# Performance work log

Measured on AMD Instinct MI355X. Metric: run time of the kernel, lower is better.

Reference implementation:

```python
import jax, jax.numpy as jnp
import numpy as np

N, E = 100000, 1600000
NODE_IN, EDGE_IN, H = 128, 16, 128


def sage_conv(x, src, dst, Wl, Wr, b, n_nodes):
    # PyG SAGEConv (aggr='mean'): out = lin_l(mean_{j->i} x_j) + lin_r(x_i), bias on lin_l
    msg_sum = jax.ops.segment_sum(x[src], dst, num_segments=n_nodes)      # [N, d]
    cnt = jax.ops.segment_sum(jnp.ones((src.shape[0],), x.dtype), dst, num_segments=n_nodes)
    mean = msg_sum / jnp.maximum(cnt, 1.0)[:, None]                        # empty neighborhoods -> 0
    return mean @ Wl + x @ Wr + b


def setup_inputs() -> dict:
    key = jax.random.key(0)
    ks = jax.random.split(key, 12)
    s = lambda d: 1.0 / np.sqrt(d)
    return {
        "x": jax.random.normal(ks[0], (N, NODE_IN), jnp.float32),
        "edge_index": jax.random.randint(ks[1], (2, E), 0, N, dtype=jnp.int64),
        "edge_attr": jax.random.normal(ks[2], (E, EDGE_IN), jnp.float32),
        "Wl1": jax.random.normal(ks[3], (NODE_IN, H), jnp.float32) * s(NODE_IN),
        "Wr1": jax.random.normal(ks[4], (NODE_IN, H), jnp.float32) * s(NODE_IN),
        "b1": jnp.zeros((H,), jnp.float32),
        "Wl2": jax.random.normal(ks[5], (H, H), jnp.float32) * s(H),
        "Wr2": jax.random.normal(ks[6], (H, H), jnp.float32) * s(H),
        "b2": jnp.zeros((H,), jnp.float32),
        "Wm1": jax.random.normal(ks[7], (2 * H + EDGE_IN, H), jnp.float32) * s(2 * H + EDGE_IN),
        "bm1": jnp.zeros((H,), jnp.float32),
        "Wm2": jax.random.normal(ks[8], (H, 1), jnp.float32) * s(H),
        "bm2": jnp.zeros((1,), jnp.float32),
    }


def reference(x, edge_index, edge_attr, Wl1, Wr1, b1, Wl2, Wr2, b2, Wm1, bm1, Wm2, bm2):
    src, dst = edge_index[0], edge_index[1]
    h = jax.nn.relu(sage_conv(x, src, dst, Wl1, Wr1, b1, N))
    h = jax.nn.relu(sage_conv(h, src, dst, Wl2, Wr2, b2, N))
    edge_feat = jnp.concatenate([h[src], h[dst], edge_attr], axis=1)  # [E, 2H+edge_in]
    out = jax.nn.relu(edge_feat @ Wm1 + bm1) @ Wm2 + bm2               # dropout is identity in eval
    return out.reshape(-1)
```

## Files before the change

kernel.cpp:

```cpp
#include <hip/hip_runtime.h>

typedef _Float16 f16;
typedef _Float16 f16x8 __attribute__((ext_vector_type(8)));
typedef float f32x4 __attribute__((ext_vector_type(4)));

#define MFMA16(a,b,c) __builtin_amdgcn_mfma_f32_16x16x32_f16((a),(b),(c),0,0,0)

__global__ void k_detect(const long long* ei, int n_nodes, int* flag) {
    long long v = ei[threadIdx.x];
    int bad = (v < 0 || v >= n_nodes);
    unsigned long long m = __ballot(bad);
    if (threadIdx.x == 0) *flag = (m == 0ULL);
}

__global__ void k_idx(const void* ei, int E, const int* __restrict__ flag,
                      int* __restrict__ src, int* __restrict__ dst) {
    int e = blockIdx.x * 256 + threadIdx.x;
    if (e >= E) return;
    if (*flag) {
        const long long* p = (const long long*)ei;
        src[e] = (int)p[e];
        dst[e] = (int)p[(size_t)E + e];
    } else {
        const int* p = (const int*)ei;
        src[e] = p[e];
        dst[e] = p[(size_t)E + e];
    }
}

__global__ void k_x2h(const float* __restrict__ x, f16* __restrict__ xh, int n) {
    int i = (blockIdx.x * 256 + threadIdx.x) * 8;
    if (i >= n) return;
    float4 a = *(const float4*)(x + i);
    float4 b = *(const float4*)(x + i + 4);
    f16x8 h;
    h[0] = (f16)a.x; h[1] = (f16)a.y; h[2] = (f16)a.z; h[3] = (f16)a.w;
    h[4] = (f16)b.x; h[5] = (f16)b.y; h[6] = (f16)b.z; h[7] = (f16)b.w;
    *(f16x8*)(xh + i) = h;
}

__global__ void k_wfrag(const float* __restrict__ Wa, const float* __restrict__ Wb,
                        f16* __restrict__ dst, int KS) {
    int t = blockIdx.x * 256 + threadIdx.x;
    int total = KS * 8 * 64;
    if (t >= total) return;
    int l = t & 63;
    int s = t >> 9;
    int k0 = s * 32 + (l >> 4) * 8;
    int j = ((t >> 6) & 7) * 16 + (l & 15);
    f16x8 h;
    #pragma unroll
    for (int e = 0; e < 8; e++) {
        int k = k0 + e;
        float v = (k < 128) ? Wa[k * 128 + j] : Wb[(k - 128) * 128 + j];
        h[e] = (f16)v;
    }
    *(f16x8*)(dst + (size_t)t * 8) = h;
}

__global__ void k_zfrag(const float* __restrict__ Wm1, f16* __restrict__ dst) {
    int t = blockIdx.x * 256 + threadIdx.x;
    if (t >= 4 * 16 * 64) return;
    int lane = t & 63, c = (t >> 6) & 15, s = t >> 10;
    int k0 = s * 32 + (lane >> 4) * 8;
    int j = c * 16 + (lane & 15);
    f16x8 h;
    #pragma unroll
    for (int e = 0; e < 8; e++) {
        int k = k0 + e;
        float v = (j < 128) ? Wm1[k * 128 + j] : Wm1[(128 + k) * 128 + (j - 128)];
        h[e] = (f16)v;
    }
    *(f16x8*)(dst + (size_t)t * 8) = h;
}

__global__ void k_wefrag(const float* __restrict__ Wm1, f16* __restrict__ dst) {
    int t = blockIdx.x * 256 + threadIdx.x;
    if (t >= 8 * 64) return;
    int lane = t & 63, ct = t >> 6;
    int k0 = (lane >> 4) * 8;
    int j = ct * 16 + (lane & 15);
    f16x8 h;
    #pragma unroll
    for (int e = 0; e < 8; e++) {
        int k = k0 + e;
        h[e] = (k < 16) ? (f16)Wm1[(256 + k) * 128 + j] : (f16)0.0f;
    }
    *(f16x8*)(dst + (size_t)t * 8) = h;
}

__global__ void k_hist(const int* __restrict__ dst, int E, int* __restrict__ deg) {
    int e = blockIdx.x * 256 + threadIdx.x;
    if (e < E) atomicAdd(&deg[dst[e]], 1);
}

__global__ void k_bsum(const int* __restrict__ deg, int n, int* __restrict__ bsum) {
    __shared__ int ws[4];
    const int tid = threadIdx.x;
    int i = blockIdx.x * 1024 + tid * 4;
    int s = 0;
    if (i + 3 < n) {
        int4 d = *(const int4*)(deg + i);
        s = d.x + d.y + d.z + d.w;
    } else {
        #pragma unroll
        for (int j = 0; j < 4; j++) if (i + j < n) s += deg[i + j];
    }
    #pragma unroll
    for (int m = 1; m < 64; m <<= 1) s += __shfl_xor(s, m, 64);
    if ((tid & 63) == 0) ws[tid >> 6] = s;
    __syncthreads();
    if (tid == 0) bsum[blockIdx.x] = ws[0] + ws[1] + ws[2] + ws[3];
}

__global__ void k_bscan(int* __restrict__ bsum, int nb, int* __restrict__ rowptr_n) {
    __shared__ int wsum[4];
    const int tid = threadIdx.x, lane = tid & 63, wid = tid >> 6;
    int v = (tid < nb) ? bsum[tid] : 0;
    int inc = v;
    #pragma unroll
    for (int off = 1; off < 64; off <<= 1) {
        int u = __shfl_up(inc, off, 64);
        if (lane >= off) inc += u;
    }
    if (lane == 63) wsum[wid] = inc;
    __syncthreads();
    int woff = 0;
    for (int j = 0; j < wid; j++) woff += wsum[j];
    int excl = woff + inc - v;
    if (tid < nb) bsum[tid] = excl;
    if (tid == nb - 1) rowptr_n[0] = excl + v;
}

__global__ void k_rowptr(const int* __restrict__ deg, int n, const int* __restrict__ boff,
                         int* __restrict__ rowptr, int* __restrict__ cursor) {
    __shared__ int wsum[4];
    const int tid = threadIdx.x, lane = tid & 63, wid = tid >> 6;
    int i = blockIdx.x * 1024 + tid * 4;
    int d0 = 0, d1 = 0, d2 = 0, d3 = 0;
    if (i + 3 < n) {
        int4 d = *(const int4*)(deg + i);
        d0 = d.x; d1 = d.y; d2 = d.z; d3 = d.w;
    } else {
        if (i     < n) d0 = deg[i];
        if (i + 1 < n) d1 = deg[i + 1];
        if (i + 2 < n) d2 = deg[i + 2];
        if (i + 3 < n) d3 = deg[i + 3];
    }
    int s = d0 + d1 + d2 + d3;
    int inc = s;
    #pragma unroll
    for (int off = 1; off < 64; off <<= 1) {
        int u = __shfl_up(inc, off, 64);
        if (lane >= off) inc += u;
    }
    if (lane == 63) wsum[wid] = inc;
    __syncthreads();
    int woff = 0;
    for (int j = 0; j < wid; j++) woff += wsum[j];
    int excl = boff[blockIdx.x] + woff + inc - s;
    int e1 = excl + d0, e2 = e1 + d1, e3 = e2 + d2;
    if (i     < n) { rowptr[i]     = excl; cursor[i]     = excl; }
    if (i + 1 < n) { rowptr[i + 1] = e1;   cursor[i + 1] = e1; }
    if (i + 2 < n) { rowptr[i + 2] = e2;   cursor[i + 2] = e2; }
    if (i + 3 < n) { rowptr[i + 3] = e3;   cursor[i + 3] = e3; }
}

__global__ void k_scatter(const int* __restrict__ src, const int* __restrict__ dst, int E,
                          int* __restrict__ cursor, int* __restrict__ col) {
    int e = blockIdx.x * 256 + threadIdx.x;
    if (e < E) {
        int p = atomicAdd(&cursor[dst[e]], 1);
        col[p] = src[e];
    }
}

#define AP 136
template<int DO_Z>
__global__ __launch_bounds__(256, DO_Z ? 3 : 4) void k_fuse(
    const f16* __restrict__ tab,
    const int* __restrict__ rowptr, const int* __restrict__ col,
    const f16* __restrict__ Wf, const float* __restrict__ bias,
    const f16* __restrict__ zwf, const float* __restrict__ bm1,
    f16* __restrict__ out, int n_rows) {
    __shared__ __align__(16) f16 sA[64 * AP];
    const int tid = threadIdx.x, lane = tid & 63, w = tid >> 6;
    const int l15 = lane & 15, g = lane >> 4;
    const int base = blockIdx.x * 64;

    const int g16 = tid >> 4, c = tid & 15;
    #pragma unroll
    for (int rep = 0; rep < 4; rep++) {
        const int node = base + rep * 16 + g16;
        float acc[8] = {0.f, 0.f, 0.f, 0.f, 0.f, 0.f, 0.f, 0.f};
        int d = 1;
        if (node < n_rows) {
            const int s0 = rowptr[node], s1 = rowptr[node + 1];
            int k = s0;
            for (; k + 3 < s1; k += 4) {
                const int n0 = col[k], n1 = col[k + 1], n2 = col[k + 2], n3 = col[k + 3];
                f16x8 v0 = *(const f16x8*)(tab + (size_t)n0 * 128 + c * 8);
                f16x8 v1 = *(const f16x8*)(tab + (size_t)n1 * 128 + c * 8);
                f16x8 v2 = *(const f16x8*)(tab + (size_t)n2 * 128 + c * 8);
                f16x8 v3 = *(const f16x8*)(tab + (size_t)n3 * 128 + c * 8);
                #pragma unroll
                for (int j = 0; j < 8; j++)
                    acc[j] += ((float)v0[j] + (float)v1[j]) + ((float)v2[j] + (float)v3[j]);
            }
            for (; k < s1; ++k) {
                const int n0 = col[k];
                f16x8 v0 = *(const f16x8*)(tab + (size_t)n0 * 128 + c * 8);
                #pragma unroll
                for (int j = 0; j < 8; j++) acc[j] += (float)v0[j];
            }
            d = s1 - s0; if (d < 1) d = 1;
        }
        const float inv = 1.f / (float)d;
        f16x8 r;
        #pragma unroll
        for (int j = 0; j < 8; j++) r[j] = (f16)(acc[j] * inv);
        *(f16x8*)&sA[(rep * 16 + g16) * AP + c * 8] = r;
    }
    __syncthreads();

    const int c0 = (2 * w) * 16 + l15, c1 = c0 + 16;
    const float b0 = bias[c0], b1 = bias[c1];
    f32x4 acc[4][2];
    #pragma unroll
    for (int t = 0; t < 4; t++) {
        acc[t][0] = f32x4{b0, b0, b0, b0};
        acc[t][1] = f32x4{b1, b1, b1, b1};
    }
    #pragma unroll
    for (int s = 0; s < 8; s++) {
        f16x8 bf0 = *(const f16x8*)&Wf[((size_t)(s * 8 + 2 * w    ) * 64 + lane) * 8];
        f16x8 bf1 = *(const f16x8*)&Wf[((size_t)(s * 8 + 2 * w + 1) * 64 + lane) * 8];
        const int koff = (s & 3) * 32 + g * 8;
        #pragma unroll
        for (int t = 0; t < 4; t++) {
            f16x8 a;
            if (s < 4) {
                a = *(const f16x8*)&sA[(t * 16 + l15) * AP + koff];
            } else {
                int row = base + t * 16 + l15;
                if (row >= n_rows) row = n_rows - 1;
                a = *(const f16x8*)(tab + (size_t)row * 128 + koff);
            }
            acc[t][0] = MFMA16(a, bf0, acc[t][0]);
            acc[t][1] = MFMA16(a, bf1, acc[t][1]);
        }
    }

    if (DO_Z == 0) {
        #pragma unroll
        for (int t = 0; t < 4; t++) {
            #pragma unroll
            for (int i = 0; i < 4; i++) {
                int row = base + t * 16 + g * 4 + i;
                if (row < n_rows) {
                    float v0 = acc[t][0][i]; v0 = v0 > 0.f ? v0 : 0.f;
                    float v1 = acc[t][1][i]; v1 = v1 > 0.f ? v1 : 0.f;
                    out[(size_t)row * 128 + c0] = (f16)v0;
                    out[(size_t)row * 128 + c1] = (f16)v1;
                }
            }
        }
    } else {
        __syncthreads();
        #pragma unroll
        for (int t = 0; t < 4; t++) {
            #pragma unroll
            for (int i = 0; i < 4; i++) {
                const int rl = t * 16 + g * 4 + i;
                float v0 = acc[t][0][i]; v0 = v0 > 0.f ? v0 : 0.f;
                float v1 = acc[t][1][i]; v1 = v1 > 0.f ? v1 : 0.f;
                sA[rl * AP + c0] = (f16)v0;
                sA[rl * AP + c1] = (f16)v1;
            }
        }
        __syncthreads();
        #pragma unroll
        for (int half = 0; half < 2; half++) {
            const int j0 = (4 * w + 2 * half) * 16 + l15, j1 = j0 + 16;
            const float zb0 = (j0 >= 128) ? bm1[j0 - 128] : 0.0f;
            const float zb1 = (j1 >= 128) ? bm1[j1 - 128] : 0.0f;
            f32x4 zacc[4][2];
            #pragma unroll
            for (int t = 0; t < 4; t++) {
                zacc[t][0] = f32x4{zb0, zb0, zb0, zb0};
                zacc[t][1] = f32x4{zb1, zb1, zb1, zb1};
            }
            #pragma unroll
            for (int s = 0; s < 4; s++) {
                f16x8 wf0 = *(const f16x8*)&zwf[((size_t)(s * 16 + 4 * w + 2 * half    ) * 64 + lane) * 8];
                f16x8 wf1 = *(const f16x8*)&zwf[((size_t)(s * 16 + 4 * w + 2 * half + 1) * 64 + lane) * 8];
                const int koff = s * 32 + g * 8;
                #pragma unroll
                for (int t = 0; t < 4; t++) {
                    f16x8 a = *(const f16x8*)&sA[(t * 16 + l15) * AP + koff];
                    zacc[t][0] = MFMA16(a, wf0, zacc[t][0]);
                    zacc[t][1] = MFMA16(a, wf1, zacc[t][1]);
                }
            }
            #pragma unroll
            for (int t = 0; t < 4; t++) {
                #pragma unroll
                for (int i = 0; i < 4; i++) {
                    int row = base + t * 16 + g * 4 + i;
                    if (row < n_rows) {
                        out[(size_t)row * 256 + j0] = (f16)zacc[t][0][i];
                        out[(size_t)row * 256 + j1] = (f16)zacc[t][1][i];
                    }
                }
            }
        }
    }
}

#define ZP 136
__global__ __launch_bounds__(256, 4) void k_edge2(
    const f16* __restrict__ z, const float* __restrict__ ea,
    const int* __restrict__ src, const int* __restrict__ dst,
    const f16* __restrict__ wef, const float* __restrict__ Wm2,
    const float* __restrict__ bm2, float* __restrict__ out,
    int E, int iters, int gridW) {
    __shared__ __align__(16) f16 sZ[64 * ZP];
    __shared__ __align__(16) f16 sEA[4 * 64 * 8];
    __shared__ float sPart[4][64];
    const int tid = threadIdx.x, lane = tid & 63, w = tid >> 6;
    const int l15 = lane & 15, g = lane >> 4;
    const int sr = lane >> 2, sq = lane & 3;
    const int slot_s = w * 16 + sr;

    for (int i = tid; i < 4 * 64; i += 256)
        *(f16x8*)(&sEA[0] + (size_t)i * 8) = f16x8{};

    const f16x8 be0 = *(const f16x8*)(wef + ((size_t)((2 * w) * 64 + lane)) * 8);
    const f16x8 be1 = *(const f16x8*)(wef + ((size_t)((2 * w + 1) * 64 + lane)) * 8);
    const float w20 = Wm2[(2 * w) * 16 + l15];
    const float w21 = Wm2[(2 * w + 1) * 16 + l15];
    const float bv = bm2[0];

    f16x8 zs[4], zd[4];
    union { f16 h[4]; uint2 u2; } eh;

    auto stage_load = [&](int ebase) {
        int er = ebase + slot_s; if (er > E - 1) er = E - 1;
        const int is = src[er], id = dst[er];
        const f16* ps = z + (size_t)is * 256 + sq * 32;
        const f16* pd = z + (size_t)id * 256 + 128 + sq * 32;
        #pragma unroll
        for (int i = 0; i < 4; i++) {
            zs[i] = *(const f16x8*)(ps + i * 8);
            zd[i] = *(const f16x8*)(pd + i * 8);
        }
        float4 ev = *(const float4*)(ea + (size_t)er * 16 + sq * 4);
        eh.h[0] = (f16)ev.x; eh.h[1] = (f16)ev.y; eh.h[2] = (f16)ev.z; eh.h[3] = (f16)ev.w;
    };
    auto stage_write = [&]() {
        f16* zp = &sZ[0] + slot_s * ZP + sq * 32;
        #pragma unroll
        for (int i = 0; i < 4; i++) {
            f16x8 v = zs[i] + zd[i];
            *(f16x8*)(zp + i * 8) = v;
        }
        f16* ep = &sEA[0] +
                  ((size_t)((slot_s >> 4) * 64 + (sq >> 1) * 16 + (slot_s & 15)) * 8 + (sq & 1) * 4);
        *(uint2*)ep = eh.u2;
    };

    stage_load(blockIdx.x * 64);
    __syncthreads();
    stage_write();
    __syncthreads();

    for (int it = 0; it < iters; ++it) {
        const int ebase = (blockIdx.x + it * gridW) * 64;
        if (ebase >= E) break;
        const int nxt = (blockIdx.x + (it + 1) * gridW) * 64;
        const bool has_next = (it + 1 < iters) && (nxt < E);
        if (has_next) stage_load(nxt);

        f32x4 acc[4][2];
        #pragma unroll
        for (int t = 0; t < 4; t++) { acc[t][0] = f32x4{0,0,0,0}; acc[t][1] = f32x4{0,0,0,0}; }
        #pragma unroll
        for (int t = 0; t < 4; t++) {
            f16x8 a = *(const f16x8*)(&sEA[0] + ((size_t)(t * 64 + lane)) * 8);
            acc[t][0] = MFMA16(a, be0, acc[t][0]);
            acc[t][1] = MFMA16(a, be1, acc[t][1]);
        }
        #pragma unroll
        for (int t = 0; t < 4; t++) {
            float p[4];
            #pragma unroll
            for (int i = 0; i < 4; i++) {
                int slot = t * 16 + g * 4 + i;
                float z0 = (float)sZ[slot * ZP + (2 * w) * 16 + l15];
                float z1 = (float)sZ[slot * ZP + (2 * w + 1) * 16 + l15];
                float v0 = z0 + acc[t][0][i]; v0 = v0 > 0.f ? v0 : 0.f;
                float v1 = z1 + acc[t][1][i]; v1 = v1 > 0.f ? v1 : 0.f;
                p[i] = v0 * w20 + v1 * w21;
            }
            #pragma unroll
            for (int m = 1; m < 16; m <<= 1)
                #pragma unroll
                for (int i = 0; i < 4; i++) p[i] += __shfl_xor(p[i], m, 64);
            if (l15 == 0)
                #pragma unroll
                for (int i = 0; i < 4; i++) sPart[w][t * 16 + g * 4 + i] = p[i];
        }
        __syncthreads();
        if (tid < 64) {
            int e = ebase + tid;
            if (e < E)
                out[e] = sPart[0][tid] + sPart[1][tid] + sPart[2][tid] + sPart[3][tid] + bv;
        }
        if (has_next) stage_write();
        __syncthreads();
    }
}

extern "C" void kernel_launch(void* const* d_in, const int* in_sizes, int n_in,
                              void* d_out, int out_size, void* d_ws, size_t ws_size,
                              hipStream_t stream) {
    const float* x   = (const float*)d_in[0];
    const void*  ei  = d_in[1];
    const float* ea  = (const float*)d_in[2];
    const float* Wl1 = (const float*)d_in[3];
    const float* Wr1 = (const float*)d_in[4];
    const float* b1  = (const float*)d_in[5];
    const float* Wl2 = (const float*)d_in[6];
    const float* Wr2 = (const float*)d_in[7];
    const float* b2  = (const float*)d_in[8];
    const float* Wm1 = (const float*)d_in[9];
    const float* bm1 = (const float*)d_in[10];
    const float* Wm2 = (const float*)d_in[11];
    const float* bm2 = (const float*)d_in[12];

    const int N = in_sizes[0] / 128;
    const int E = in_sizes[1] / 2;

    char* ws = (char*)d_ws;
    size_t off = 0;
    auto alloc = [&](size_t bytes) -> void* {
        void* p = ws + off;
        off = (off + bytes + 255) & ~(size_t)255;
        return p;
    };
    f16* z      = (f16*)alloc((size_t)N * 256 * 2);
    f16* xh     = z;
    f16* h1     = (f16*)alloc((size_t)N * 128 * 2);
    int* src    = (int*)alloc((size_t)E * 4);
    int* dst    = (int*)alloc((size_t)E * 4);
    int* col    = (int*)alloc((size_t)E * 4);
    int* deg    = (int*)alloc((size_t)N * 4);
    int* rowptr = (int*)alloc((size_t)(N + 1) * 4);
    int* cursor = (int*)alloc((size_t)N * 4);
    int* bsum   = (int*)alloc((size_t)1024 * 4);
    f16* w1f    = (f16*)alloc((size_t)8 * 8 * 64 * 8 * 2);
    f16* w2f    = (f16*)alloc((size_t)8 * 8 * 64 * 8 * 2);
    f16* zwf    = (f16*)alloc((size_t)4 * 16 * 64 * 8 * 2);
    f16* wef    = (f16*)alloc((size_t)8 * 64 * 8 * 2);
    int* flag   = (int*)alloc(4);
    if (off > ws_size) return;

    const int eb = (E + 255) / 256;
    const int nbk = (N + 1023) / 1024;
    const int rb64 = (N + 63) / 64;

    k_detect<<<1, 64, 0, stream>>>((const long long*)ei, N, flag);
    k_idx<<<eb, 256, 0, stream>>>(ei, E, flag, src, dst);
    k_x2h<<<(N * 128 / 8 + 255) / 256, 256, 0, stream>>>(x, xh, N * 128);
    k_wfrag<<<16, 256, 0, stream>>>(Wl1, Wr1, w1f, 8);
    k_wfrag<<<16, 256, 0, stream>>>(Wl2, Wr2, w2f, 8);
    k_zfrag<<<16, 256, 0, stream>>>(Wm1, zwf);
    k_wefrag<<<2, 256, 0, stream>>>(Wm1, wef);

    hipMemsetAsync(deg, 0, (size_t)N * 4, stream);
    k_hist<<<eb, 256, 0, stream>>>(dst, E, deg);
    k_bsum<<<nbk, 256, 0, stream>>>(deg, N, bsum);
    k_bscan<<<1, 256, 0, stream>>>(bsum, nbk, rowptr + N);
    k_rowptr<<<nbk, 256, 0, stream>>>(deg, N, bsum, rowptr, cursor);
    k_scatter<<<eb, 256, 0, stream>>>(src, dst, E, cursor, col);

    k_fuse<0><<<rb64, 256, 0, stream>>>(xh, rowptr, col, w1f, b1, nullptr, nullptr, h1, N);
    k_fuse<1><<<rb64, 256, 0, stream>>>(h1, rowptr, col, w2f, b2, zwf, bm1, z, N);

    const int eg = 1792;
    const int nb = (E + 63) / 64;
    const int e_iters = (nb + eg - 1) / eg;
    k_edge2<<<eg, 256, 0, stream>>>(z, ea, src, dst, wef, Wm2, bm2,
                                    (float*)d_out, E, e_iters, eg);
}
```

Measured before the change: 570.8 us.

## Split aggregation from GEMM and use chunked column-slab layout for node features

Node features are stored as 8 column slabs of 16 halves ([chunk][N][16]) instead of row-major 128-wide rows. Neighbor aggregation becomes its own kernel that handles one slab per block, so each pass gathers from a 3.2 MB slab that can stay cache-resident rather than a full 25.6 MB table. The SAGE GEMMs then read the mean and self features from the slab layout. This adds a mean buffer, extra kernel launches and a round trip of the mean through global memory, and makes the self-feature A-loads 32-byte strided pieces.

Measured after the change: 608.9 us. 6.7% more time.

```diff
diff --git a/kernel.cpp b/kernel.cpp
--- a/kernel.cpp
+++ b/kernel.cpp
@@ -5,6 +5,7 @@
 typedef float f32x4 __attribute__((ext_vector_type(4)));
 
 #define MFMA16(a,b,c) __builtin_amdgcn_mfma_f32_16x16x32_f16((a),(b),(c),0,0,0)
+
 
 __global__ void k_detect(const long long* ei, int n_nodes, int* flag) {
     long long v = ei[threadIdx.x];
@@ -28,15 +29,18 @@
     }
 }
 
-__global__ void k_x2h(const float* __restrict__ x, f16* __restrict__ xh, int n) {
-    int i = (blockIdx.x * 256 + threadIdx.x) * 8;
-    if (i >= n) return;
-    float4 a = *(const float4*)(x + i);
-    float4 b = *(const float4*)(x + i + 4);
+__global__ void k_x2h(const float* __restrict__ x, f16* __restrict__ xs, int N) {
+    int i = blockIdx.x * 256 + threadIdx.x;
+    if (i >= N * 16) return;
+    int n = i >> 4, cg = i & 15;
+    const float* px = x + (size_t)n * 128 + cg * 8;
+    float4 a = *(const float4*)px;
+    float4 b = *(const float4*)(px + 4);
     f16x8 h;
     h[0] = (f16)a.x; h[1] = (f16)a.y; h[2] = (f16)a.z; h[3] = (f16)a.w;
     h[4] = (f16)b.x; h[5] = (f16)b.y; h[6] = (f16)b.z; h[7] = (f16)b.w;
-    *(f16x8*)(xh + i) = h;
+    int chunk = cg >> 1, off = (cg & 1) * 8;
+    *(f16x8*)(xs + ((size_t)chunk * N + n) * 16 + off) = h;
 }
 
 __global__ void k_wfrag(const float* __restrict__ Wa, const float* __restrict__ Wb,
@@ -175,56 +179,101 @@
     }
 }
 
+__global__ __launch_bounds__(256) void k_aggs(
+    const f16* __restrict__ tabs, const int* __restrict__ rowptr,
+    const int* __restrict__ col, f16* __restrict__ means, int N) {
+    const int chunk = blockIdx.x & 7;
+    const int tile = blockIdx.x >> 3;
+    const int team = threadIdx.x >> 1, half = threadIdx.x & 1;
+    const int node = tile * 128 + team;
+    if (node >= N) return;
+    const f16* slab = tabs + (size_t)chunk * N * 16 + half * 8;
+    const int s0 = rowptr[node], s1 = rowptr[node + 1];
+    float acc[8] = {0.f, 0.f, 0.f, 0.f, 0.f, 0.f, 0.f, 0.f};
+    int k = s0;
+    for (; k + 3 < s1; k += 4) {
+        const int n0 = col[k], n1 = col[k + 1], n2 = col[k + 2], n3 = col[k + 3];
+        f16x8 v0 = *(const f16x8*)(slab + (size_t)n0 * 16);
+        f16x8 v1 = *(const f16x8*)(slab + (size_t)n1 * 16);
+        f16x8 v2 = *(const f16x8*)(slab + (size_t)n2 * 16);
+        f16x8 v3 = *(const f16x8*)(slab + (size_t)n3 * 16);
+        #pragma unroll
+        for (int j = 0; j < 8; j++)
+            acc[j] += ((float)v0[j] + (float)v1[j]) + ((float)v2[j] + (float)v3[j]);
+    }
+    for (; k < s1; ++k) {
+        const int n0 = col[k];
+        f16x8 v0 = *(const f16x8*)(slab + (size_t)n0 * 16);
+        #pragma unroll
+        for (int j = 0; j < 8; j++) acc[j] += (float)v0[j];
+    }
+    int d = s1 - s0; if (d < 1) d = 1;
+    const float inv = 1.f / (float)d;
+    f16x8 r;
+    #pragma unroll
+    for (int j = 0; j < 8; j++) r[j] = (f16)(acc[j] * inv);
+    *(f16x8*)(means + ((size_t)chunk * N + node) * 16 + half * 8) = r;
+}
+
+__global__ __launch_bounds__(256) void k_gemm2(
+    const f16* __restrict__ As, const f16* __restrict__ Ss,
+    const f16* __restrict__ Wf, const float* __restrict__ bias,
+    f16* __restrict__ outs, int N) {
+    const int tid = threadIdx.x, lane = tid & 63, w = tid >> 6;
+    const int l15 = lane & 15, g = lane >> 4;
+    const int base = blockIdx.x * 64;
+    const int c0 = (2 * w) * 16 + l15, c1 = c0 + 16;
+    const float b0 = bias[c0], b1 = bias[c1];
+    const int chp = g >> 1, off = (g & 1) * 8;
+    f32x4 acc[4][2];
+    #pragma unroll
+    for (int t = 0; t < 4; t++) {
+        acc[t][0] = f32x4{b0, b0, b0, b0};
+        acc[t][1] = f32x4{b1, b1, b1, b1};
+    }
+    #pragma unroll
+    for (int s = 0; s < 8; s++) {
+        f16x8 bf0 = *(const f16x8*)&Wf[((size_t)(s * 8 + 2 * w    ) * 64 + lane) * 8];
+        f16x8 bf1 = *(const f16x8*)&Wf[((size_t)(s * 8 + 2 * w + 1) * 64 + lane) * 8];
+        const f16* Asrc = (s < 4) ? As : Ss;
+        const int chunk = (s & 3) * 2 + chp;
+        #pragma unroll
+        for (int t = 0; t < 4; t++) {
+            int row = base + t * 16 + l15;
+            if (row >= N) row = N - 1;
+            f16x8 a = *(const f16x8*)(Asrc + ((size_t)chunk * N + row) * 16 + off);
+            acc[t][0] = MFMA16(a, bf0, acc[t][0]);
+            acc[t][1] = MFMA16(a, bf1, acc[t][1]);
+        }
+    }
+    #pragma unroll
+    for (int t = 0; t < 4; t++) {
+        #pragma unroll
+        for (int i = 0; i < 4; i++) {
+            int row = base + t * 16 + g * 4 + i;
+            if (row < N) {
+                float v0 = acc[t][0][i]; v0 = v0 > 0.f ? v0 : 0.f;
+                float v1 = acc[t][1][i]; v1 = v1 > 0.f ? v1 : 0.f;
+                outs[((size_t)(2 * w    ) * N + row) * 16 + l15] = (f16)v0;
+                outs[((size_t)(2 * w + 1) * N + row) * 16 + l15] = (f16)v1;
+            }
+        }
+    }
+}
+
 #define AP 136
-template<int DO_Z>
-__global__ __launch_bounds__(256, DO_Z ? 3 : 4) void k_fuse(
-    const f16* __restrict__ tab,
-    const int* __restrict__ rowptr, const int* __restrict__ col,
+__global__ __launch_bounds__(256, 3) void k_gemmz(
+    const f16* __restrict__ As, const f16* __restrict__ Ss,
     const f16* __restrict__ Wf, const float* __restrict__ bias,
     const f16* __restrict__ zwf, const float* __restrict__ bm1,
-    f16* __restrict__ out, int n_rows) {
+    f16* __restrict__ z, int N) {
     __shared__ __align__(16) f16 sA[64 * AP];
     const int tid = threadIdx.x, lane = tid & 63, w = tid >> 6;
     const int l15 = lane & 15, g = lane >> 4;
     const int base = blockIdx.x * 64;
-
-    const int g16 = tid >> 4, c = tid & 15;
-    #pragma unroll
-    for (int rep = 0; rep < 4; rep++) {
-        const int node = base + rep * 16 + g16;
-        float acc[8] = {0.f, 0.f, 0.f, 0.f, 0.f, 0.f, 0.f, 0.f};
-        int d = 1;
-        if (node < n_rows) {
-            const int s0 = rowptr[node], s1 = rowptr[node + 1];
-            int k = s0;
-            for (; k + 3 < s1; k += 4) {
-                const int n0 = col[k], n1 = col[k + 1], n2 = col[k + 2], n3 = col[k + 3];
-                f16x8 v0 = *(const f16x8*)(tab + (size_t)n0 * 128 + c * 8);
-                f16x8 v1 = *(const f16x8*)(tab + (size_t)n1 * 128 + c * 8);
-                f16x8 v2 = *(const f16x8*)(tab + (size_t)n2 * 128 + c * 8);
-                f16x8 v3 = *(const f16x8*)(tab + (size_t)n3 * 128 + c * 8);
-                #pragma unroll
-                for (int j = 0; j < 8; j++)
-                    acc[j] += ((float)v0[j] + (float)v1[j]) + ((float)v2[j] + (float)v3[j]);
-            }
-            for (; k < s1; ++k) {
-                const int n0 = col[k];
-                f16x8 v0 = *(const f16x8*)(tab + (size_t)n0 * 128 + c * 8);
-                #pragma unroll
-                for (int j = 0; j < 8; j++) acc[j] += (float)v0[j];
-            }
-            d = s1 - s0; if (d < 1) d = 1;
-        }
-        const float inv = 1.f / (float)d;
-        f16x8 r;
-        #pragma unroll
-        for (int j = 0; j < 8; j++) r[j] = (f16)(acc[j] * inv);
-        *(f16x8*)&sA[(rep * 16 + g16) * AP + c * 8] = r;
-    }
-    __syncthreads();
-
     const int c0 = (2 * w) * 16 + l15, c1 = c0 + 16;
     const float b0 = bias[c0], b1 = bias[c1];
+    const int chp = g >> 1, off = (g & 1) * 8;
     f32x4 acc[4][2];
     #pragma unroll
     for (int t = 0; t < 4; t++) {
@@ -235,82 +284,60 @@
     for (int s = 0; s < 8; s++) {
         f16x8 bf0 = *(const f16x8*)&Wf[((size_t)(s * 8 + 2 * w    ) * 64 + lane) * 8];
         f16x8 bf1 = *(const f16x8*)&Wf[((size_t)(s * 8 + 2 * w + 1) * 64 + lane) * 8];
-        const int koff = (s & 3) * 32 + g * 8;
+        const f16* Asrc = (s < 4) ? As : Ss;
+        const int chunk = (s & 3) * 2 + chp;
         #pragma unroll
         for (int t = 0; t < 4; t++) {
-            f16x8 a;
-            if (s < 4) {
-                a = *(const f16x8*)&sA[(t * 16 + l15) * AP + koff];
-            } else {
-                int row = base + t * 16 + l15;
-                if (row >= n_rows) row = n_rows - 1;
-                a = *(const f16x8*)(tab + (size_t)row * 128 + koff);
-            }
+            int row = base + t * 16 + l15;
+            if (row >= N) row = N - 1;
+            f16x8 a = *(const f16x8*)(Asrc + ((size_t)chunk * N + row) * 16 + off);
             acc[t][0] = MFMA16(a, bf0, acc[t][0]);
             acc[t][1] = MFMA16(a, bf1, acc[t][1]);
         }
     }
-
-    if (DO_Z == 0) {
+    #pragma unroll
+    for (int t = 0; t < 4; t++) {
+        #pragma unroll
+        for (int i = 0; i < 4; i++) {
+            const int rl = t * 16 + g * 4 + i;
+            float v0 = acc[t][0][i]; v0 = v0 > 0.f ? v0 : 0.f;
+            float v1 = acc[t][1][i]; v1 = v1 > 0.f ? v1 : 0.f;
+            sA[rl * AP + c0] = (f16)v0;
+            sA[rl * AP + c1] = (f16)v1;
+        }
+    }
+    __syncthreads();
+    #pragma unroll
+    for (int half = 0; half < 2; half++) {
+        const int j0 = (4 * w + 2 * half) * 16 + l15, j1 = j0 + 16;
+        const float zb0 = (j0 >= 128) ? bm1[j0 - 128] : 0.0f;
+        const float zb1 = (j1 >= 128) ? bm1[j1 - 128] : 0.0f;
+        f32x4 zacc[4][2];
+        #pragma unroll
+        for (int t = 0; t < 4; t++) {
+            zacc[t][0] = f32x4{zb0, zb0, zb0, zb0};
+            zacc[t][1] = f32x4{zb1, zb1, zb1, zb1};
+        }
+        #pragma unroll
+        for (int s = 0; s < 4; s++) {
+            f16x8 wf0 = *(const f16x8*)&zwf[((size_t)(s * 16 + 4 * w + 2 * half    ) * 64 + lane) * 8];
+            f16x8 wf1 = *(const f16x8*)&zwf[((size_t)(s * 16 + 4 * w + 2 * half + 1) * 64 + lane) * 8];
+            const int koff = s * 32 + g * 8;
+            #pragma unroll
+            for (int t = 0; t < 4; t++) {
+                f16x8 a = *(const f16x8*)&sA[(t * 16 + l15) * AP + koff];
+                zacc[t][0] = MFMA16(a, wf0, zacc[t][0]);
+                zacc[t][1] = MFMA16(a, wf1, zacc[t][1]);
+            }
+        }
         #pragma unroll
         for (int t = 0; t < 4; t++) {
             #pragma unroll
             for (int i = 0; i < 4; i++) {
                 int row = base + t * 16 + g * 4 + i;
-                if (row < n_rows) {
-                    float v0 = acc[t][0][i]; v0 = v0 > 0.f ? v0 : 0.f;
-                    float v1 = acc[t][1][i]; v1 = v1 > 0.f ? v1 : 0.f;
-                    out[(size_t)row * 128 + c0] = (f16)v0;
-                    out[(size_t)row * 128 + c1] = (f16)v1;
-                }
-            }
-        }
-    } else {
-        __syncthreads();
-        #pragma unroll
-        for (int t = 0; t < 4; t++) {
-            #pragma unroll
-            for (int i = 0; i < 4; i++) {
-                const int rl = t * 16 + g * 4 + i;
-                float v0 = acc[t][0][i]; v0 = v0 > 0.f ? v0 : 0.f;
-                float v1 = acc[t][1][i]; v1 = v1 > 0.f ? v1 : 0.f;
-                sA[rl * AP + c0] = (f16)v0;
-                sA[rl * AP + c1] = (f16)v1;
-            }
-        }
-        __syncthreads();
-        #pragma unroll
-        for (int half = 0; half < 2; half++) {
-            const int j0 = (4 * w + 2 * half) * 16 + l15, j1 = j0 + 16;
-            const float zb0 = (j0 >= 128) ? bm1[j0 - 128] : 0.0f;
-            const float zb1 = (j1 >= 128) ? bm1[j1 - 128] : 0.0f;
-            f32x4 zacc[4][2];
-            #pragma unroll
-            for (int t = 0; t < 4; t++) {
-                zacc[t][0] = f32x4{zb0, zb0, zb0, zb0};
-                zacc[t][1] = f32x4{zb1, zb1, zb1, zb1};
-            }
-            #pragma unroll
-            for (int s = 0; s < 4; s++) {
-                f16x8 wf0 = *(const f16x8*)&zwf[((size_t)(s * 16 + 4 * w + 2 * half    ) * 64 + lane) * 8];
-                f16x8 wf1 = *(const f16x8*)&zwf[((size_t)(s * 16 + 4 * w + 2 * half + 1) * 64 + lane) * 8];
-                const int koff = s * 32 + g * 8;
-                #pragma unroll
-                for (int t = 0; t < 4; t++) {
-                    f16x8 a = *(const f16x8*)&sA[(t * 16 + l15) * AP + koff];
-                    zacc[t][0] = MFMA16(a, wf0, zacc[t][0]);
-                    zacc[t][1] = MFMA16(a, wf1, zacc[t][1]);
-                }
-            }
-            #pragma unroll
-            for (int t = 0; t < 4; t++) {
-                #pragma unroll
-                for (int i = 0; i < 4; i++) {
-                    int row = base + t * 16 + g * 4 + i;
-                    if (row < n_rows) {
-                        out[(size_t)row * 256 + j0] = (f16)zacc[t][0][i];
-                        out[(size_t)row * 256 + j1] = (f16)zacc[t][1][i];
-                    }
+                if (row < N) {
+                    z[(size_t)row * 256 + j0] = (f16)zacc[t][0][i];
+                    z[(size_t)row * 256 + j1] = (f16)zacc[t][1][i];
                 }
             }
         }
@@ -451,6 +478,7 @@
     f16* z      = (f16*)alloc((size_t)N * 256 * 2);
     f16* xh     = z;
     f16* h1     = (f16*)alloc((size_t)N * 128 * 2);
+    f16* mean   = (f16*)alloc((size_t)N * 128 * 2);
     int* src    = (int*)alloc((size_t)E * 4);
     int* dst    = (int*)alloc((size_t)E * 4);
     int* col    = (int*)alloc((size_t)E * 4);
@@ -471,7 +499,7 @@
 
     k_detect<<<1, 64, 0, stream>>>((const long long*)ei, N, flag);
     k_idx<<<eb, 256, 0, stream>>>(ei, E, flag, src, dst);
-    k_x2h<<<(N * 128 / 8 + 255) / 256, 256, 0, stream>>>(x, xh, N * 128);
+    k_x2h<<<(N * 16 + 255) / 256, 256, 0, stream>>>(x, xh, N);
     k_wfrag<<<16, 256, 0, stream>>>(Wl1, Wr1, w1f, 8);
     k_wfrag<<<16, 256, 0, stream>>>(Wl2, Wr2, w2f, 8);
     k_zfrag<<<16, 256, 0, stream>>>(Wm1, zwf);
@@ -484,8 +512,12 @@
     k_rowptr<<<nbk, 256, 0, stream>>>(deg, N, bsum, rowptr, cursor);
     k_scatter<<<eb, 256, 0, stream>>>(src, dst, E, cursor, col);
 
-    k_fuse<0><<<rb64, 256, 0, stream>>>(xh, rowptr, col, w1f, b1, nullptr, nullptr, h1, N);
-    k_fuse<1><<<rb64, 256, 0, stream>>>(h1, rowptr, col, w2f, b2, zwf, bm1, z, N);
+    const int ag = 8 * ((N + 127) / 128);
+
+    k_aggs<<<ag, 256, 0, stream>>>(xh, rowptr, col, mean, N);
+    k_gemm2<<<rb64, 256, 0, stream>>>(mean, xh, w1f, b1, h1, N);
+    k_aggs<<<ag, 256, 0, stream>>>(h1, rowptr, col, mean, N);
+    k_gemmz<<<rb64, 256, 0, stream>>>(mean, h1, w2f, b2, zwf, bm1, z, N);
 
     const int eg = 1792;
     const int nb = (E + 63) / 64;
```

## Process edges in CSR (dst-sorted) order in edge MLP, then permute outputs

Applied to the files above, without the earlier changes.

The edge MLP kernel now walks edges in the dst-sorted CSR order built by the scatter pass, so consecutive edges share destination rows of z and hit cache better. The scatter pass records the original edge id and destination per slot, and a new permutation kernel writes results back to original order. The degree histogram is also folded into the index conversion kernel, dropping one launch and one read of dst. In exchange, edge_attr reads become gathers, and the change adds extra index arrays, a temporary output buffer and a scattered write pass.

Result: faster. 559.1 us (-2.1%).

```diff
diff --git a/kernel.cpp b/kernel.cpp
--- a/kernel.cpp
+++ b/kernel.cpp
@@ -14,18 +14,23 @@
 }
 
 __global__ void k_idx(const void* ei, int E, const int* __restrict__ flag,
-                      int* __restrict__ src, int* __restrict__ dst) {
+                      int* __restrict__ src, int* __restrict__ dst,
+                      int* __restrict__ deg) {
     int e = blockIdx.x * 256 + threadIdx.x;
     if (e >= E) return;
+    int s, d;
     if (*flag) {
         const long long* p = (const long long*)ei;
-        src[e] = (int)p[e];
-        dst[e] = (int)p[(size_t)E + e];
+        s = (int)p[e];
+        d = (int)p[(size_t)E + e];
     } else {
         const int* p = (const int*)ei;
-        src[e] = p[e];
-        dst[e] = p[(size_t)E + e];
-    }
+        s = p[e];
+        d = p[(size_t)E + e];
+    }
+    src[e] = s;
+    dst[e] = d;
+    atomicAdd(&deg[d], 1);
 }
 
 __global__ void k_x2h(const float* __restrict__ x, f16* __restrict__ xh, int n) {
@@ -87,11 +92,6 @@
         h[e] = (k < 16) ? (f16)Wm1[(256 + k) * 128 + j] : (f16)0.0f;
     }
     *(f16x8*)(dst + (size_t)t * 8) = h;
-}
-
-__global__ void k_hist(const int* __restrict__ dst, int E, int* __restrict__ deg) {
-    int e = blockIdx.x * 256 + threadIdx.x;
-    if (e < E) atomicAdd(&deg[dst[e]], 1);
 }
 
 __global__ void k_bsum(const int* __restrict__ deg, int n, int* __restrict__ bsum) {
@@ -167,11 +167,15 @@
 }
 
 __global__ void k_scatter(const int* __restrict__ src, const int* __restrict__ dst, int E,
-                          int* __restrict__ cursor, int* __restrict__ col) {
+                          int* __restrict__ cursor, int* __restrict__ col,
+                          int* __restrict__ eid, int* __restrict__ dstp) {
     int e = blockIdx.x * 256 + threadIdx.x;
     if (e < E) {
-        int p = atomicAdd(&cursor[dst[e]], 1);
+        int d = dst[e];
+        int p = atomicAdd(&cursor[d], 1);
         col[p] = src[e];
+        eid[p] = e;
+        dstp[p] = d;
     }
 }
 
@@ -320,9 +324,9 @@
 #define ZP 136
 __global__ __launch_bounds__(256, 4) void k_edge2(
     const f16* __restrict__ z, const float* __restrict__ ea,
-    const int* __restrict__ src, const int* __restrict__ dst,
+    const int* __restrict__ colp, const int* __restrict__ dstp, const int* __restrict__ eidp,
     const f16* __restrict__ wef, const float* __restrict__ Wm2,
-    const float* __restrict__ bm2, float* __restrict__ out,
+    const float* __restrict__ bm2, float* __restrict__ tmp,
     int E, int iters, int gridW) {
     __shared__ __align__(16) f16 sZ[64 * ZP];
     __shared__ __align__(16) f16 sEA[4 * 64 * 8];
@@ -344,9 +348,9 @@
     f16x8 zs[4], zd[4];
     union { f16 h[4]; uint2 u2; } eh;
 
-    auto stage_load = [&](int ebase) {
-        int er = ebase + slot_s; if (er > E - 1) er = E - 1;
-        const int is = src[er], id = dst[er];
+    auto stage_load = [&](int pbase) {
+        int pr = pbase + slot_s; if (pr > E - 1) pr = E - 1;
+        const int is = colp[pr], id = dstp[pr], ee = eidp[pr];
         const f16* ps = z + (size_t)is * 256 + sq * 32;
         const f16* pd = z + (size_t)id * 256 + 128 + sq * 32;
         #pragma unroll
@@ -354,7 +358,7 @@
             zs[i] = *(const f16x8*)(ps + i * 8);
             zd[i] = *(const f16x8*)(pd + i * 8);
         }
-        float4 ev = *(const float4*)(ea + (size_t)er * 16 + sq * 4);
+        float4 ev = *(const float4*)(ea + (size_t)ee * 16 + sq * 4);
         eh.h[0] = (f16)ev.x; eh.h[1] = (f16)ev.y; eh.h[2] = (f16)ev.z; eh.h[3] = (f16)ev.w;
     };
     auto stage_write = [&]() {
@@ -375,8 +379,8 @@
     __syncthreads();
 
     for (int it = 0; it < iters; ++it) {
-        const int ebase = (blockIdx.x + it * gridW) * 64;
-        if (ebase >= E) break;
+        const int pbase = (blockIdx.x + it * gridW) * 64;
+        if (pbase >= E) break;
         const int nxt = (blockIdx.x + (it + 1) * gridW) * 64;
         const bool has_next = (it + 1 < iters) && (nxt < E);
         if (has_next) stage_load(nxt);
@@ -412,13 +416,19 @@
         }
         __syncthreads();
         if (tid < 64) {
-            int e = ebase + tid;
-            if (e < E)
-                out[e] = sPart[0][tid] + sPart[1][tid] + sPart[2][tid] + sPart[3][tid] + bv;
+            int p = pbase + tid;
+            if (p < E)
+                tmp[p] = sPart[0][tid] + sPart[1][tid] + sPart[2][tid] + sPart[3][tid] + bv;
         }
         if (has_next) stage_write();
         __syncthreads();
     }
+}
+
+__global__ void k_perm(const float* __restrict__ tmp, const int* __restrict__ eidp,
+                       float* __restrict__ out, int E) {
+    int p = blockIdx.x * 256 + threadIdx.x;
+    if (p < E) out[eidp[p]] = tmp[p];
 }
 
 extern "C" void kernel_launch(void* const* d_in, const int* in_sizes, int n_in,
@@ -454,6 +464,9 @@
     int* src    = (int*)alloc((size_t)E * 4);
     int* dst    = (int*)alloc((size_t)E * 4);
     int* col    = (int*)alloc((size_t)E * 4);
+    int* eid    = (int*)alloc((size_t)E * 4);
+    int* dstp   = (int*)alloc((size_t)E * 4);
+    float* tmp  = (float*)alloc((size_t)E * 4);
     int* deg    = (int*)alloc((size_t)N * 4);
     int* rowptr = (int*)alloc((size_t)(N + 1) * 4);
     int* cursor = (int*)alloc((size_t)N * 4);
@@ -470,19 +483,18 @@
     const int rb64 = (N + 63) / 64;
 
     k_detect<<<1, 64, 0, stream>>>((const long long*)ei, N, flag);
-    k_idx<<<eb, 256, 0, stream>>>(ei, E, flag, src, dst);
+    hipMemsetAsync(deg, 0, (size_t)N * 4, stream);
+    k_idx<<<eb, 256, 0, stream>>>(ei, E, flag, src, dst, deg);
     k_x2h<<<(N * 128 / 8 + 255) / 256, 256, 0, stream>>>(x, xh, N * 128);
     k_wfrag<<<16, 256, 0, stream>>>(Wl1, Wr1, w1f, 8);
     k_wfrag<<<16, 256, 0, stream>>>(Wl2, Wr2, w2f, 8);
     k_zfrag<<<16, 256, 0, stream>>>(Wm1, zwf);
     k_wefrag<<<2, 256, 0, stream>>>(Wm1, wef);
 
-    hipMemsetAsync(deg, 0, (size_t)N * 4, stream);
-    k_hist<<<eb, 256, 0, stream>>>(dst, E, deg);
     k_bsum<<<nbk, 256, 0, stream>>>(deg, N, bsum);
     k_bscan<<<1, 256, 0, stream>>>(bsum, nbk, rowptr + N);
     k_rowptr<<<nbk, 256, 0, stream>>>(deg, N, bsum, rowptr, cursor);
-    k_scatter<<<eb, 256, 0, stream>>>(src, dst, E, cursor, col);
+    k_scatter<<<eb, 256, 0, stream>>>(src, dst, E, cursor, col, eid, dstp);
 
     k_fuse<0><<<rb64, 256, 0, stream>>>(xh, rowptr, col, w1f, b1, nullptr, nullptr, h1, N);
     k_fuse<1><<<rb64, 256, 0, stream>>>(h1, rowptr, col, w2f, b2, zwf, bm1, z, N);
@@ -490,6 +502,7 @@
     const int eg = 1792;
     const int nb = (E + 63) / 64;
     const int e_iters = (nb + eg - 1) / eg;
-    k_edge2<<<eg, 256, 0, stream>>>(z, ea, src, dst, wef, Wm2, bm2,
-                                    (float*)d_out, E, e_iters, eg);
-}
+    k_edge2<<<eg, 256, 0, stream>>>(z, ea, col, dstp, eid, wef, Wm2, bm2,
+                                    tmp, E, e_iters, eg);
+    k_perm<<<eb, 256, 0, stream>>>(tmp, eid, (float*)d_out, E);
+}
```
